# Kernel tuning notes

Measured on AMD Instinct MI355X. Metric: run time of the kernel, lower is better.

The kernel has to match this reference:

```python
import jax, jax.numpy as jnp
import numpy as np
import math

NEG_INF = -1e30  # stand-in for float('-inf'); softmax/logsumexp treat it identically


def _fnoise(x):
    # factorized NoisyNet transform f(x) = sign(x) * sqrt(|x|)
    return jnp.sign(x) * jnp.sqrt(jnp.abs(x))


def setup_inputs() -> dict:
    B, T, D, E = 4, 4096, 2048, 16
    key = jax.random.key(0)
    ks = jax.random.split(key, 6)
    sigma_init = 0.4 / math.sqrt(D)  # sigma_zero / sqrt(in_features)
    return {
        "mh_output": jax.random.normal(ks[0], (B, T, D), dtype=jnp.float32),
        "weight": jax.random.normal(ks[1], (E, D), dtype=jnp.float32) * 0.02,
        "sigma_weight": jnp.full((E, D), sigma_init, dtype=jnp.float32),
        "bias": jax.random.normal(ks[2], (E,), dtype=jnp.float32) * 0.02,
        "sigma_bias": jnp.full((E,), sigma_init, dtype=jnp.float32),
        "eps_in": jax.random.normal(ks[3], (D,), dtype=jnp.float32),
        "eps_out": jax.random.normal(ks[4], (E,), dtype=jnp.float32),
    }


def reference(mh_output, weight, sigma_weight, bias, sigma_bias, eps_in, eps_out):
    top_k = 2
    E = weight.shape[0]

    # NoisyFactorizedLinear: W' = W + sigma_W * (f(eps_out) f(eps_in)^T)
    f_in = _fnoise(eps_in)            # [D]
    f_out = _fnoise(eps_out)          # [E]
    w_noisy = weight + sigma_weight * (f_out[:, None] * f_in[None, :])  # [E, D]
    b_noisy = bias + sigma_bias * f_out                                 # [E]
    logits = jnp.einsum("btd,ed->bte", mh_output, w_noisy) + b_noisy    # [B,T,E]
    # dropout(p=0.125) is identity in eval mode

    top_vals, indices = jax.lax.top_k(logits, top_k)                    # [B,T,k]
    # scatter top-k back into a -inf-filled tensor == mask of selected experts
    keep = jnp.sum(jax.nn.one_hot(indices, E, dtype=jnp.bool_), axis=-2)  # [B,T,E]
    sparse_logits = jnp.where(keep, logits, NEG_INF)

    router_output = jax.nn.softmax(sparse_logits, axis=-1)

    # z-loss: mean(logsumexp(sparse_logits, -1)^2); only top-k entries survive
    lse = jax.scipy.special.logsumexp(top_vals, axis=-1)                # [B,T]
    z_loss = jnp.mean(lse ** 2)

    return router_output, indices, z_loss
```

## Files before the change

kernel.cpp:

```cpp
#include <hip/hip_runtime.h>
#include <math.h>

#define NROWS 16384
#define DDIM  2048
#define NEXP  16
#define RBLOCKS 512
#define WPB 8
#define ZN (RBLOCKS * WPB)

__device__ __forceinline__ float fnoise(float x) {
    return copysignf(sqrtf(fabsf(x)), x);
}

__device__ __forceinline__ void async_copy16(const float4* g, float4* l) {
    __builtin_amdgcn_global_load_lds(
        (const __attribute__((address_space(1))) void*)g,
        (__attribute__((address_space(3))) void*)l, 16, 0, 0);
}


__global__ void prep_kernel(const float* __restrict__ weight,
                            const float* __restrict__ sigma_weight,
                            const float* __restrict__ bias,
                            const float* __restrict__ sigma_bias,
                            const float* __restrict__ eps_in,
                            const float* __restrict__ eps_out,
                            float* __restrict__ w_noisy,
                            float* __restrict__ b_noisy) {
    int idx = blockIdx.x * blockDim.x + threadIdx.x;
    int e = idx >> 11;
    int d = idx & (DDIM - 1);
    float fi = fnoise(eps_in[d]);
    float fo = fnoise(eps_out[e]);
    w_noisy[idx] = weight[idx] + sigma_weight[idx] * fo * fi;
    if (idx < NEXP) {
        b_noisy[idx] = bias[idx] + sigma_bias[idx] * fnoise(eps_out[idx]);
    }
}

__global__ __launch_bounds__(512, 4) void router_kernel(
        const float* __restrict__ x,
        const float* __restrict__ w_noisy,
        const float* __restrict__ b_noisy,
        float* __restrict__ out_router,
        float* __restrict__ out_idx,
        float* __restrict__ zpart) {
    __shared__ float4 wlds[2][NEXP * 128];

    const int tid  = threadIdx.x;
    const int wv   = tid >> 6;
    const int lane = tid & 63;

    const int rowBase = blockIdx.x * 32 + wv * 4;
    const float4* xr0 = (const float4*)(x + (size_t)(rowBase + 0) * DDIM);
    const float4* xr1 = (const float4*)(x + (size_t)(rowBase + 1) * DDIM);
    const float4* xr2 = (const float4*)(x + (size_t)(rowBase + 2) * DDIM);
    const float4* xr3 = (const float4*)(x + (size_t)(rowBase + 3) * DDIM);
    const float4* wsrc = (const float4*)w_noisy;

    float acc[64];
    #pragma unroll
    for (int i = 0; i < 64; ++i) acc[i] = 0.0f;

    float4 xbuf[2][4];

    #pragma unroll
    for (int j = 0; j < 4; ++j) {
        int fb = j * 512 + wv * 64;
        async_copy16(wsrc + (size_t)(fb >> 7) * 512 + (fb & 127) + lane,
                     &wlds[0][fb]);
    }
    xbuf[0][0] = xr0[lane];
    xbuf[0][1] = xr1[lane];
    xbuf[0][2] = xr2[lane];
    xbuf[0][3] = xr3[lane];
    __syncthreads();

    #pragma unroll
    for (int q = 0; q < 4; ++q) {
        const int cb = q & 1;
        const int nb = cb ^ 1;
        if (q < 3) {
            #pragma unroll
            for (int j = 0; j < 4; ++j) {
                int fb = j * 512 + wv * 64;
                async_copy16(wsrc + (size_t)(fb >> 7) * 512 + (q + 1) * 128
                                 + (fb & 127) + lane,
                             &wlds[nb][fb]);
            }
        }
        #pragma unroll
        for (int h = 0; h < 2; ++h) {
            const int c = 2 * q + h;
            const int xc = c & 1;
            const int xn = xc ^ 1;
            if (c < 7) {
                int p = (c + 1) * 64 + lane;
                xbuf[xn][0] = xr0[p];
                xbuf[xn][1] = xr1[p];
                xbuf[xn][2] = xr2[p];
                xbuf[xn][3] = xr3[p];
            }
            #pragma unroll
            for (int e = 0; e < 16; ++e) {
                float4 w = wlds[cb][e * 128 + h * 64 + lane];
                float s0 = acc[0 * 16 + e];
                float s1 = acc[1 * 16 + e];
                float s2 = acc[2 * 16 + e];
                float s3 = acc[3 * 16 + e];
                s0 = fmaf(xbuf[xc][0].x, w.x, s0); s0 = fmaf(xbuf[xc][0].y, w.y, s0);
                s0 = fmaf(xbuf[xc][0].z, w.z, s0); s0 = fmaf(xbuf[xc][0].w, w.w, s0);
                s1 = fmaf(xbuf[xc][1].x, w.x, s1); s1 = fmaf(xbuf[xc][1].y, w.y, s1);
                s1 = fmaf(xbuf[xc][1].z, w.z, s1); s1 = fmaf(xbuf[xc][1].w, w.w, s1);
                s2 = fmaf(xbuf[xc][2].x, w.x, s2); s2 = fmaf(xbuf[xc][2].y, w.y, s2);
                s2 = fmaf(xbuf[xc][2].z, w.z, s2); s2 = fmaf(xbuf[xc][2].w, w.w, s2);
                s3 = fmaf(xbuf[xc][3].x, w.x, s3); s3 = fmaf(xbuf[xc][3].y, w.y, s3);
                s3 = fmaf(xbuf[xc][3].z, w.z, s3); s3 = fmaf(xbuf[xc][3].w, w.w, s3);
                acc[0 * 16 + e] = s0;
                acc[1 * 16 + e] = s1;
                acc[2 * 16 + e] = s2;
                acc[3 * 16 + e] = s3;
            }
        }
        if (q < 3) __syncthreads();
    }

    #pragma unroll
    for (int half = 32; half >= 1; half >>= 1) {
        #pragma unroll
        for (int i = 0; i < half; ++i) {
            bool hi = (lane & half) != 0;
            float keep = hi ? acc[i + half] : acc[i];
            float send = hi ? acc[i] : acc[i + half];
            float recv = __shfl_xor(send, half, 64);
            acc[i] = keep + recv;
        }
    }

    const int e = lane & 15;
    const int r = lane >> 4;
    const int row = rowBase + r;
    float logit = acc[0] + b_noisy[e];

    float m1 = logit; int i1 = e;
    #pragma unroll
    for (int off = 8; off >= 1; off >>= 1) {
        float om = __shfl_xor(m1, off, 64);
        int   oi = __shfl_xor(i1, off, 64);
        if (om > m1 || (om == m1 && oi < i1)) { m1 = om; i1 = oi; }
    }
    float v2 = (e == i1) ? -3.4e38f : logit;
    float m2 = v2; int i2 = e;
    #pragma unroll
    for (int off = 8; off >= 1; off >>= 1) {
        float om = __shfl_xor(m2, off, 64);
        int   oi = __shfl_xor(i2, off, 64);
        if (om > m2 || (om == m2 && oi < i2)) { m2 = om; i2 = oi; }
    }

    float t = expf(m2 - m1);
    float p1 = 1.0f / (1.0f + t);
    float val = (e == i1) ? p1 : ((e == i2) ? t * p1 : 0.0f);
    out_router[(size_t)rowBase * NEXP + lane] = val;

    if (e < 2) {
        out_idx[(size_t)row * 2 + e] = (float)((e == 0) ? i1 : i2);
    }

    float zv = 0.0f;
    if (e == 0) {
        float lse = m1 + log1pf(t);
        zv = lse * lse;
    }
    zv += __shfl_xor(zv, 16, 64);
    zv += __shfl_xor(zv, 32, 64);
    if (lane == 0) {
        zpart[blockIdx.x * WPB + wv] = zv;
    }
}

__global__ void finalize_kernel(const float* __restrict__ zpart,
                                float* __restrict__ out) {
    __shared__ float ws4[4];
    int tid = threadIdx.x;
    float s = 0.0f;
    for (int i = tid; i < ZN; i += 256) s += zpart[i];
    #pragma unroll
    for (int off = 32; off >= 1; off >>= 1) s += __shfl_xor(s, off, 64);
    if ((tid & 63) == 0) ws4[tid >> 6] = s;
    __syncthreads();
    if (tid == 0) {
        float total = ws4[0] + ws4[1] + ws4[2] + ws4[3];
        out[NROWS * NEXP + NROWS * 2] = total * (1.0f / (float)NROWS);
    }
}

extern "C" void kernel_launch(void* const* d_in, const int* in_sizes, int n_in,
                              void* d_out, int out_size, void* d_ws, size_t ws_size,
                              hipStream_t stream) {
    const float* mh      = (const float*)d_in[0];
    const float* weight  = (const float*)d_in[1];
    const float* sigw    = (const float*)d_in[2];
    const float* bias    = (const float*)d_in[3];
    const float* sigb    = (const float*)d_in[4];
    const float* eps_in  = (const float*)d_in[5];
    const float* eps_out = (const float*)d_in[6];

    float* out      = (float*)d_out;
    float* w_noisy  = (float*)d_ws;
    float* b_noisy  = w_noisy + NEXP * DDIM;
    float* zpart    = w_noisy + 32800;

    prep_kernel<<<(NEXP * DDIM) / 256, 256, 0, stream>>>(
        weight, sigw, bias, sigb, eps_in, eps_out, w_noisy, b_noisy);

    router_kernel<<<RBLOCKS, 512, 0, stream>>>(
        mh, w_noisy, b_noisy, out, out + NROWS * NEXP, zpart);

    finalize_kernel<<<1, 256, 0, stream>>>(zpart, out);
}
```

Measured before the change: 211.0 us.

## Read noisy weights directly from global memory instead of LDS double-buffering

The router kernel no longer stages the 128 KB noisy weight matrix through double-buffered LDS with async global-to-LDS copies and barriers. Each wave now loads its weight float4s straight from global memory, relying on L1/L2 caching since every block reads the same small matrix. This removes LDS traffic and __syncthreads stalls but makes weight reads depend on cache hit rates and global load latency. The prep kernel is also vectorised to float4 with fewer blocks.

Measured after the change: 254.4 us. 20.6% more time.

```diff
diff --git a/kernel.cpp b/kernel.cpp
--- a/kernel.cpp
+++ b/kernel.cpp
@@ -10,12 +10,6 @@
 
 __device__ __forceinline__ float fnoise(float x) {
     return copysignf(sqrtf(fabsf(x)), x);
-}
-
-__device__ __forceinline__ void async_copy16(const float4* g, float4* l) {
-    __builtin_amdgcn_global_load_lds(
-        (const __attribute__((address_space(1))) void*)g,
-        (__attribute__((address_space(3))) void*)l, 16, 0, 0);
 }
 
 
@@ -27,14 +21,29 @@
                             const float* __restrict__ eps_out,
                             float* __restrict__ w_noisy,
                             float* __restrict__ b_noisy) {
-    int idx = blockIdx.x * blockDim.x + threadIdx.x;
-    int e = idx >> 11;
-    int d = idx & (DDIM - 1);
-    float fi = fnoise(eps_in[d]);
+    int gid = blockIdx.x * blockDim.x + threadIdx.x;
+    int e  = gid >> 9;
+    int c4 = gid & 511;
+    float4 w  = ((const float4*)weight)[gid];
+    float4 sw = ((const float4*)sigma_weight)[gid];
+    float4 ei = ((const float4*)eps_in)[c4];
     float fo = fnoise(eps_out[e]);
-    w_noisy[idx] = weight[idx] + sigma_weight[idx] * fo * fi;
-    if (idx < NEXP) {
-        b_noisy[idx] = bias[idx] + sigma_bias[idx] * fnoise(eps_out[idx]);
+    float4 r;
+    r.x = w.x + sw.x * fo * fnoise(ei.x);
+    r.y = w.y + sw.y * fo * fnoise(ei.y);
+    r.z = w.z + sw.z * fo * fnoise(ei.z);
+    r.w = w.w + sw.w * fo * fnoise(ei.w);
+    ((float4*)w_noisy)[gid] = r;
+    if (gid < 4) {
+        float4 b  = ((const float4*)bias)[gid];
+        float4 sb = ((const float4*)sigma_bias)[gid];
+        float4 eo = ((const float4*)eps_out)[gid];
+        float4 rb;
+        rb.x = b.x + sb.x * fnoise(eo.x);
+        rb.y = b.y + sb.y * fnoise(eo.y);
+        rb.z = b.z + sb.z * fnoise(eo.z);
+        rb.w = b.w + sb.w * fnoise(eo.w);
+        ((float4*)b_noisy)[gid] = rb;
     }
 }
 
@@ -45,8 +54,6 @@
         float* __restrict__ out_router,
         float* __restrict__ out_idx,
         float* __restrict__ zpart) {
-    __shared__ float4 wlds[2][NEXP * 128];
-
     const int tid  = threadIdx.x;
     const int wv   = tid >> 6;
     const int lane = tid & 63;
@@ -63,66 +70,42 @@
     for (int i = 0; i < 64; ++i) acc[i] = 0.0f;
 
     float4 xbuf[2][4];
-
-    #pragma unroll
-    for (int j = 0; j < 4; ++j) {
-        int fb = j * 512 + wv * 64;
-        async_copy16(wsrc + (size_t)(fb >> 7) * 512 + (fb & 127) + lane,
-                     &wlds[0][fb]);
-    }
     xbuf[0][0] = xr0[lane];
     xbuf[0][1] = xr1[lane];
     xbuf[0][2] = xr2[lane];
     xbuf[0][3] = xr3[lane];
-    __syncthreads();
-
-    #pragma unroll
-    for (int q = 0; q < 4; ++q) {
-        const int cb = q & 1;
-        const int nb = cb ^ 1;
-        if (q < 3) {
-            #pragma unroll
-            for (int j = 0; j < 4; ++j) {
-                int fb = j * 512 + wv * 64;
-                async_copy16(wsrc + (size_t)(fb >> 7) * 512 + (q + 1) * 128
-                                 + (fb & 127) + lane,
-                             &wlds[nb][fb]);
-            }
+
+    #pragma unroll
+    for (int c = 0; c < 8; ++c) {
+        const int xc = c & 1;
+        const int xn = xc ^ 1;
+        if (c < 7) {
+            int p = (c + 1) * 64 + lane;
+            xbuf[xn][0] = xr0[p];
+            xbuf[xn][1] = xr1[p];
+            xbuf[xn][2] = xr2[p];
+            xbuf[xn][3] = xr3[p];
         }
         #pragma unroll
-        for (int h = 0; h < 2; ++h) {
-            const int c = 2 * q + h;
-            const int xc = c & 1;
-            const int xn = xc ^ 1;
-            if (c < 7) {
-                int p = (c + 1) * 64 + lane;
-                xbuf[xn][0] = xr0[p];
-                xbuf[xn][1] = xr1[p];
-                xbuf[xn][2] = xr2[p];
-                xbuf[xn][3] = xr3[p];
-            }
-            #pragma unroll
-            for (int e = 0; e < 16; ++e) {
-                float4 w = wlds[cb][e * 128 + h * 64 + lane];
-                float s0 = acc[0 * 16 + e];
-                float s1 = acc[1 * 16 + e];
-                float s2 = acc[2 * 16 + e];
-                float s3 = acc[3 * 16 + e];
-                s0 = fmaf(xbuf[xc][0].x, w.x, s0); s0 = fmaf(xbuf[xc][0].y, w.y, s0);
-                s0 = fmaf(xbuf[xc][0].z, w.z, s0); s0 = fmaf(xbuf[xc][0].w, w.w, s0);
-                s1 = fmaf(xbuf[xc][1].x, w.x, s1); s1 = fmaf(xbuf[xc][1].y, w.y, s1);
-                s1 = fmaf(xbuf[xc][1].z, w.z, s1); s1 = fmaf(xbuf[xc][1].w, w.w, s1);
-                s2 = fmaf(xbuf[xc][2].x, w.x, s2); s2 = fmaf(xbuf[xc][2].y, w.y, s2);
-                s2 = fmaf(xbuf[xc][2].z, w.z, s2); s2 = fmaf(xbuf[xc][2].w, w.w, s2);
-                s3 = fmaf(xbuf[xc][3].x, w.x, s3); s3 = fmaf(xbuf[xc][3].y, w.y, s3);
-                s3 = fmaf(xbuf[xc][3].z, w.z, s3); s3 = fmaf(xbuf[xc][3].w, w.w, s3);
-                acc[0 * 16 + e] = s0;
-                acc[1 * 16 + e] = s1;
-                acc[2 * 16 + e] = s2;
-                acc[3 * 16 + e] = s3;
-            }
+        for (int e = 0; e < 16; ++e) {
+            float4 w = wsrc[e * 512 + c * 64 + lane];
+            float s0 = acc[0 * 16 + e];
+            float s1 = acc[1 * 16 + e];
+            float s2 = acc[2 * 16 + e];
+            float s3 = acc[3 * 16 + e];
+            s0 = fmaf(xbuf[xc][0].x, w.x, s0); s0 = fmaf(xbuf[xc][0].y, w.y, s0);
+            s0 = fmaf(xbuf[xc][0].z, w.z, s0); s0 = fmaf(xbuf[xc][0].w, w.w, s0);
+            s1 = fmaf(xbuf[xc][1].x, w.x, s1); s1 = fmaf(xbuf[xc][1].y, w.y, s1);
+            s1 = fmaf(xbuf[xc][1].z, w.z, s1); s1 = fmaf(xbuf[xc][1].w, w.w, s1);
+            s2 = fmaf(xbuf[xc][2].x, w.x, s2); s2 = fmaf(xbuf[xc][2].y, w.y, s2);
+            s2 = fmaf(xbuf[xc][2].z, w.z, s2); s2 = fmaf(xbuf[xc][2].w, w.w, s2);
+            s3 = fmaf(xbuf[xc][3].x, w.x, s3); s3 = fmaf(xbuf[xc][3].y, w.y, s3);
+            s3 = fmaf(xbuf[xc][3].z, w.z, s3); s3 = fmaf(xbuf[xc][3].w, w.w, s3);
+            acc[0 * 16 + e] = s0;
+            acc[1 * 16 + e] = s1;
+            acc[2 * 16 + e] = s2;
+            acc[3 * 16 + e] = s3;
         }
-        if (q < 3) __syncthreads();
     }
 
     #pragma unroll
@@ -211,7 +194,7 @@
     float* b_noisy  = w_noisy + NEXP * DDIM;
     float* zpart    = w_noisy + 32800;
 
-    prep_kernel<<<(NEXP * DDIM) / 256, 256, 0, stream>>>(
+    prep_kernel<<<32, 256, 0, stream>>>(
         weight, sigw, bias, sigb, eps_in, eps_out, w_noisy, b_noisy);
 
     router_kernel<<<RBLOCKS, 512, 0, stream>>>(
```
